# Kernel optimization log

Measured on AMD Instinct MI355X. Metric: run time of the kernel, lower is better.

Reference implementation:

```python
import jax, jax.numpy as jnp
import numpy as np

B, C, H, W = 8, 768, 32, 32
NH = 12
HD = C // NH
HID = 4 * C
EPS = 1e-5


def _layer_norm(x, g, b):
    mu = jnp.mean(x, axis=-1, keepdims=True)
    var = jnp.mean(jnp.square(x - mu), axis=-1, keepdims=True)
    return (x - mu) * jax.lax.rsqrt(var + EPS) * g + b


def setup_inputs() -> dict:
    key = jax.random.key(0)
    ks = jax.random.split(key, 12)
    s = 0.02
    return {
        "x": jax.random.normal(ks[0], (B, C, H, W), jnp.float32),
        "conv_w": jax.random.normal(ks[1], (C, 1, 3, 3), jnp.float32) * s,  # depthwise OIHW
        "conv_b": jnp.zeros((C,), jnp.float32),
        "ln1_g": jnp.ones((C,), jnp.float32),
        "ln1_b": jnp.zeros((C,), jnp.float32),
        "qkv_w": jax.random.normal(ks[2], (3 * C, C), jnp.float32) * s,  # no bias (qkv_bias=False)
        "proj_w": jax.random.normal(ks[3], (C, C), jnp.float32) * s,
        "proj_b": jnp.zeros((C,), jnp.float32),
        "ln2_g": jnp.ones((C,), jnp.float32),
        "ln2_b": jnp.zeros((C,), jnp.float32),
        "fc1_w": jax.random.normal(ks[4], (HID, C), jnp.float32) * s,
        "fc1_b": jnp.zeros((HID,), jnp.float32),
        "fc2_w": jax.random.normal(ks[5], (C, HID), jnp.float32) * s,
        "fc2_b": jnp.zeros((C,), jnp.float32),
    }


def reference(x, conv_w, conv_b, ln1_g, ln1_b, qkv_w, proj_w, proj_b,
              ln2_g, ln2_b, fc1_w, fc1_b, fc2_w, fc2_b):
    # depthwise 3x3 conv positional embedding, residual
    pe = jax.lax.conv_general_dilated(
        x, conv_w, window_strides=(1, 1), padding=((1, 1), (1, 1)),
        dimension_numbers=("NCHW", "OIHW", "NCHW"), feature_group_count=C)
    x = x + pe + conv_b[None, :, None, None]

    b, c, h, w = x.shape
    t = x.reshape(b, c, h * w).transpose(0, 2, 1)  # [B, N, C]

    # attention
    hn = _layer_norm(t, ln1_g, ln1_b)
    qkv = hn @ qkv_w.T  # [B, N, 3C]
    qkv = qkv.reshape(b, h * w, 3, NH, HD).transpose(2, 0, 3, 1, 4)  # [3, B, nh, N, hd]
    q, k, v = qkv[0], qkv[1], qkv[2]
    scale = HD ** -0.5
    attn = jax.nn.softmax(jnp.einsum("bhnd,bhmd->bhnm", q, k) * scale, axis=-1)
    o = jnp.einsum("bhnm,bhmd->bhnd", attn, v).transpose(0, 2, 1, 3).reshape(b, h * w, c)
    t = t + (o @ proj_w.T + proj_b)

    # MLP
    hn = _layer_norm(t, ln2_g, ln2_b)
    hid = jax.nn.gelu(hn @ fc1_w.T + fc1_b, approximate=False)
    t = t + (hid @ fc2_w.T + fc2_b)

    return t.transpose(0, 2, 1).reshape(b, c, h, w)
```

## Files before the change

### kernel.cpp

```cpp
#include <hip/hip_runtime.h>
#include <math.h>


typedef __bf16 bf16;
typedef __attribute__((ext_vector_type(8))) __bf16 bf16x8;
typedef __attribute__((ext_vector_type(4))) __bf16 bf16x4;
typedef __attribute__((ext_vector_type(4))) float f32x4;

#define B_   8
#define C_   768
#define N_   1024
#define NH_  12
#define HD_  64
#define HID_ 3072
#define NTOK   (B_ * N_)
#define NHEADS (B_ * NH_)
#define FA_C   0.1803368801111601f

__device__ __forceinline__ void gload_lds16(const void* g, void* l) {
  __builtin_amdgcn_global_load_lds(
      (__attribute__((address_space(1))) void*)(void*)g,
      (__attribute__((address_space(3))) void*)l, 16, 0, 0);
}

__device__ __forceinline__ float gelu1(float x) {
  float u = 0.7978845608028654f * x * (1.0f + 0.044715f * x * x);
  float e = __builtin_amdgcn_exp2f(u * 2.885390081777927f);
  float th = 1.0f - 2.0f * __builtin_amdgcn_rcpf(e + 1.0f);
  return 0.5f * x * (1.0f + th);
}

#define PIPE_SYNC(N)                                              \
  do {                                                            \
    asm volatile("s_waitcnt vmcnt(" #N ") lgkmcnt(0)" ::: "memory"); \
    __builtin_amdgcn_sched_barrier(0);                            \
    __builtin_amdgcn_s_barrier();                                 \
    __builtin_amdgcn_sched_barrier(0);                            \
    asm volatile("" ::: "memory");                                \
  } while (0)

__global__ __launch_bounds__(512) void gemm_fc1(
    const bf16* __restrict__ A, const bf16* __restrict__ Bw,
    const float* __restrict__ bias, bf16* __restrict__ outp,
    int K, int lda, int ldb, int ntiles, int mtpx, int ldo) {
  __shared__ __align__(16) char smem[114688];
  const int tid = threadIdx.x;
  const int wave = tid >> 6, lane = tid & 63;
  const int wr = wave & 1, wc = wave >> 1;
  const int lr = lane & 15, kq = lane >> 4;

  const int bid = blockIdx.x;
  const int g = bid & 7, s = bid >> 3;
  const int ms = s / ntiles;
  const int m0 = (g * mtpx + ms) * 256;
  const int n0 = (s - ms * ntiles) * 192;

  f32x4 acc[8][3];
#pragma unroll
  for (int i = 0; i < 8; ++i)
#pragma unroll
    for (int j = 0; j < 3; ++j) acc[i][j] = (f32x4){0.f, 0.f, 0.f, 0.f};

  const bf16* pa[4];
  const bf16* pb[3];
  int da[4], db[3];
#pragma unroll
  for (int c = 0; c < 4; ++c) {
    const int sidx = c * 512 + tid;
    const int r = sidx >> 3, seg = (sidx & 7) ^ (r & 7);
    pa[c] = A + (size_t)(m0 + r) * lda + seg * 8;
    da[c] = sidx * 16;
  }
#pragma unroll
  for (int c = 0; c < 3; ++c) {
    const int sidx = c * 512 + tid;
    const int r = sidx >> 3, seg = (sidx & 7) ^ (r & 7);
    pb[c] = Bw + (size_t)(n0 + r) * ldb + seg * 8;
    db[c] = 32768 + sidx * 16;
  }

  const int NT = K >> 6;

  gload_lds16(pb[0], smem + db[0]);
  gload_lds16(pb[1], smem + db[1]);
  gload_lds16(pb[2], smem + db[2]);
  gload_lds16(pa[0], smem + da[0]);
  gload_lds16(pa[1], smem + da[1]);
  gload_lds16(pa[2], smem + da[2]);
  gload_lds16(pa[3], smem + da[3]);
#pragma unroll
  for (int c = 0; c < 4; ++c) pa[c] += 64;
#pragma unroll
  for (int c = 0; c < 3; ++c) pb[c] += 64;

  for (int t = 0; t < NT - 1; ++t) {
    const char* rb = smem + (t & 1) * 57344;
    char* wb = smem + ((t & 1) ^ 1) * 57344;
    bf16x8 af[4], bf0[3], bf1[3];

    PIPE_SYNC(1);
#pragma unroll
    for (int i = 0; i < 4; ++i) {
      const int r = wr * 128 + i * 16 + lr;
      af[i] = *(const bf16x8*)(rb + (r * 8 + (kq ^ (r & 7))) * 16);
    }
#pragma unroll
    for (int j = 0; j < 3; ++j) {
      const int r = wc * 48 + j * 16 + lr;
      bf0[j] = *(const bf16x8*)(rb + 32768 + (r * 8 + (kq ^ (r & 7))) * 16);
    }
    gload_lds16(pb[0], wb + db[0]); pb[0] += 64;
    gload_lds16(pb[1], wb + db[1]); pb[1] += 64;
    __builtin_amdgcn_s_setprio(1);
#pragma unroll
    for (int i = 0; i < 4; ++i)
#pragma unroll
      for (int j = 0; j < 3; ++j)
        acc[i][j] = __builtin_amdgcn_mfma_f32_16x16x32_bf16(bf0[j], af[i],
                                                            acc[i][j], 0, 0, 0);
    __builtin_amdgcn_s_setprio(0);

    PIPE_SYNC(2);
#pragma unroll
    for (int i = 0; i < 4; ++i) {
      const int r = wr * 128 + 64 + i * 16 + lr;
      af[i] = *(const bf16x8*)(rb + (r * 8 + (kq ^ (r & 7))) * 16);
    }
    gload_lds16(pb[2], wb + db[2]); pb[2] += 64;
    gload_lds16(pa[0], wb + da[0]); pa[0] += 64;
    __builtin_amdgcn_s_setprio(1);
#pragma unroll
    for (int i = 0; i < 4; ++i)
#pragma unroll
      for (int j = 0; j < 3; ++j)
        acc[4 + i][j] = __builtin_amdgcn_mfma_f32_16x16x32_bf16(
            bf0[j], af[i], acc[4 + i][j], 0, 0, 0);
    __builtin_amdgcn_s_setprio(0);

    PIPE_SYNC(4);
#pragma unroll
    for (int i = 0; i < 4; ++i) {
      const int r = wr * 128 + i * 16 + lr;
      af[i] = *(const bf16x8*)(rb + (r * 8 + ((4 + kq) ^ (r & 7))) * 16);
    }
#pragma unroll
    for (int j = 0; j < 3; ++j) {
      const int r = wc * 48 + j * 16 + lr;
      bf1[j] = *(const bf16x8*)(rb + 32768 + (r * 8 + ((4 + kq) ^ (r & 7))) * 16);
    }
    gload_lds16(pa[1], wb + da[1]); pa[1] += 64;
    gload_lds16(pa[2], wb + da[2]); pa[2] += 64;
    __builtin_amdgcn_s_setprio(1);
#pragma unroll
    for (int i = 0; i < 4; ++i)
#pragma unroll
      for (int j = 0; j < 3; ++j)
        acc[i][j] = __builtin_amdgcn_mfma_f32_16x16x32_bf16(bf1[j], af[i],
                                                            acc[i][j], 0, 0, 0);
    __builtin_amdgcn_s_setprio(0);

    PIPE_SYNC(6);
#pragma unroll
    for (int i = 0; i < 4; ++i) {
      const int r = wr * 128 + 64 + i * 16 + lr;
      af[i] = *(const bf16x8*)(rb + (r * 8 + ((4 + kq) ^ (r & 7))) * 16);
    }
    gload_lds16(pa[3], wb + da[3]); pa[3] += 64;
    __builtin_amdgcn_s_setprio(1);
#pragma unroll
    for (int i = 0; i < 4; ++i)
#pragma unroll
      for (int j = 0; j < 3; ++j)
        acc[4 + i][j] = __builtin_amdgcn_mfma_f32_16x16x32_bf16(
            bf1[j], af[i], acc[4 + i][j], 0, 0, 0);
    __builtin_amdgcn_s_setprio(0);
  }

  {
    const char* rb = smem + ((NT - 1) & 1) * 57344;
    bf16x8 af[4], bf0[3], bf1[3];
    PIPE_SYNC(0);
#pragma unroll
    for (int j = 0; j < 3; ++j) {
      const int r = wc * 48 + j * 16 + lr;
      bf0[j] = *(const bf16x8*)(rb + 32768 + (r * 8 + (kq ^ (r & 7))) * 16);
      bf1[j] = *(const bf16x8*)(rb + 32768 + (r * 8 + ((4 + kq) ^ (r & 7))) * 16);
    }
    __builtin_amdgcn_s_setprio(1);
#pragma unroll
    for (int half = 0; half < 2; ++half) {
#pragma unroll
      for (int i = 0; i < 4; ++i) {
        const int r = wr * 128 + half * 64 + i * 16 + lr;
        af[i] = *(const bf16x8*)(rb + (r * 8 + (kq ^ (r & 7))) * 16);
      }
#pragma unroll
      for (int i = 0; i < 4; ++i)
#pragma unroll
        for (int j = 0; j < 3; ++j)
          acc[half * 4 + i][j] = __builtin_amdgcn_mfma_f32_16x16x32_bf16(
              bf0[j], af[i], acc[half * 4 + i][j], 0, 0, 0);
#pragma unroll
      for (int i = 0; i < 4; ++i) {
        const int r = wr * 128 + half * 64 + i * 16 + lr;
        af[i] = *(const bf16x8*)(rb + (r * 8 + ((4 + kq) ^ (r & 7))) * 16);
      }
#pragma unroll
      for (int i = 0; i < 4; ++i)
#pragma unroll
        for (int j = 0; j < 3; ++j)
          acc[half * 4 + i][j] = __builtin_amdgcn_mfma_f32_16x16x32_bf16(
              bf1[j], af[i], acc[half * 4 + i][j], 0, 0, 0);
    }
    __builtin_amdgcn_s_setprio(0);
  }

#pragma unroll
  for (int j = 0; j < 3; ++j) {
    const int n = n0 + wc * 48 + j * 16 + kq * 4;
    const f32x4 bv = *(const f32x4*)(bias + n);
#pragma unroll
    for (int i = 0; i < 8; ++i) {
      const int m = m0 + wr * 128 + i * 16 + lr;
      const f32x4 v = acc[i][j];
      bf16x4 pk = {(bf16)gelu1(v[0] + bv[0]), (bf16)gelu1(v[1] + bv[1]),
                   (bf16)gelu1(v[2] + bv[2]), (bf16)gelu1(v[3] + bv[3])};
      *(bf16x4*)(outp + (size_t)m * ldo + n) = pk;
    }
  }
}

__global__ __launch_bounds__(512) void gemm_fc2(
    const bf16* __restrict__ A, const bf16* __restrict__ Bw,
    const float* __restrict__ bias, const float* __restrict__ resid,
    float* __restrict__ outp, int K, int lda, int ldb) {
  __shared__ __align__(16) char smem[122880];
  const int tid = threadIdx.x;
  const int wave = tid >> 6, lane = tid & 63;
  const int wr = wave & 1, wc = wave >> 1;
  const int lr = lane & 15, kq = lane >> 4;

  const int bid = blockIdx.x;
  const int g = bid & 7, s = bid >> 3;
  const int ms = s >> 2;
  const int m0 = (g * 8 + ms) * 128;
  const int n0 = (s & 3) * 192;

  f32x4 acc[4][3];
#pragma unroll
  for (int i = 0; i < 4; ++i)
#pragma unroll
    for (int j = 0; j < 3; ++j) acc[i][j] = (f32x4){0.f, 0.f, 0.f, 0.f};

  const bf16* pa[2];
  const bf16* pb[3];
  int da[2], db[3];
#pragma unroll
  for (int c = 0; c < 2; ++c) {
    const int sidx = c * 512 + tid;
    const int r = sidx >> 3, seg = (sidx & 7) ^ (r & 7);
    pa[c] = A + (size_t)(m0 + r) * lda + seg * 8;
    da[c] = sidx * 16;
  }
#pragma unroll
  for (int c = 0; c < 3; ++c) {
    const int sidx = c * 512 + tid;
    const int r = sidx >> 3, seg = (sidx & 7) ^ (r & 7);
    pb[c] = Bw + (size_t)(n0 + r) * ldb + seg * 8;
    db[c] = 16384 + sidx * 16;
  }

  const int NT = K >> 6;

#pragma unroll
  for (int tt = 0; tt < 2; ++tt) {
    char* wb = smem + tt * 40960;
    gload_lds16(pb[0], wb + db[0]);
    gload_lds16(pb[1], wb + db[1]);
    gload_lds16(pb[2], wb + db[2]);
    gload_lds16(pa[0], wb + da[0]);
    gload_lds16(pa[1], wb + da[1]);
    pb[0] += 64; pb[1] += 64; pb[2] += 64; pa[0] += 64; pa[1] += 64;
  }

  int cur = 0;
  for (int t = 0; t < NT - 1; ++t) {
    const char* rb = smem + cur * 40960;
    PIPE_SYNC(5);
    if (t < NT - 2) {
      int wi = cur + 2; if (wi >= 3) wi -= 3;
      char* wb = smem + wi * 40960;
      gload_lds16(pb[0], wb + db[0]); pb[0] += 64;
      gload_lds16(pb[1], wb + db[1]); pb[1] += 64;
      gload_lds16(pb[2], wb + db[2]); pb[2] += 64;
      gload_lds16(pa[0], wb + da[0]); pa[0] += 64;
      gload_lds16(pa[1], wb + da[1]); pa[1] += 64;
    }
    bf16x8 af[4], bf[3];
#pragma unroll
// ... 13 lines not shown
      for (int j = 0; j < 3; ++j)
        acc[i][j] = __builtin_amdgcn_mfma_f32_16x16x32_bf16(bf[j], af[i],
                                                            acc[i][j], 0, 0, 0);
    __builtin_amdgcn_s_setprio(0);
#pragma unroll
    for (int i = 0; i < 4; ++i) {
      const int r = wr * 64 + i * 16 + lr;
      af[i] = *(const bf16x8*)(rb + (r * 8 + ((4 + kq) ^ (r & 7))) * 16);
    }
#pragma unroll
    for (int j = 0; j < 3; ++j) {
      const int r = wc * 48 + j * 16 + lr;
      bf[j] = *(const bf16x8*)(rb + 16384 + (r * 8 + ((4 + kq) ^ (r & 7))) * 16);
    }
    __builtin_amdgcn_s_setprio(1);
#pragma unroll
    for (int i = 0; i < 4; ++i)
#pragma unroll
      for (int j = 0; j < 3; ++j)
        acc[i][j] = __builtin_amdgcn_mfma_f32_16x16x32_bf16(bf[j], af[i],
                                                            acc[i][j], 0, 0, 0);
    __builtin_amdgcn_s_setprio(0);
    if (++cur == 3) cur = 0;
  }

  {
    const char* rb = smem + cur * 40960;
    bf16x8 af[4], bf[3];
    PIPE_SYNC(0);
#pragma unroll
    for (int kh = 0; kh < 2; ++kh) {
      const int c0 = kh * 4 + kq;
#pragma unroll
      for (int i = 0; i < 4; ++i) {
        const int r = wr * 64 + i * 16 + lr;
        af[i] = *(const bf16x8*)(rb + (r * 8 + (c0 ^ (r & 7))) * 16);
      }
#pragma unroll
      for (int j = 0; j < 3; ++j) {
        const int r = wc * 48 + j * 16 + lr;
        bf[j] = *(const bf16x8*)(rb + 16384 + (r * 8 + (c0 ^ (r & 7))) * 16);
      }
      __builtin_amdgcn_s_setprio(1);
#pragma unroll
      for (int i = 0; i < 4; ++i)
#pragma unroll
        for (int j = 0; j < 3; ++j)
          acc[i][j] = __builtin_amdgcn_mfma_f32_16x16x32_bf16(bf[j], af[i],
                                                              acc[i][j], 0, 0, 0);
      __builtin_amdgcn_s_setprio(0);
    }
  }

  {
    float* tile = (float*)smem;
    const int b = m0 >> 10, tok0 = m0 & (N_ - 1);
#pragma unroll
    for (int sl = 0; sl < 3; ++sl) {
      __syncthreads();
#pragma unroll
      for (int j = 0; j < 3; ++j) {
        const int nl0 = wc * 48 + j * 16 + kq * 4;
        if (((wc * 48 + j * 16) >> 6) == sl) {
          const int n = n0 + nl0;
          const f32x4 bv = *(const f32x4*)(bias + n);
#pragma unroll
          for (int i = 0; i < 4; ++i) {
            const int ml = wr * 64 + i * 16 + lr;
            const float* rp = resid + (size_t)(m0 + ml) * C_ + n;
            f32x4 old = *(const f32x4*)rp;
            const f32x4 v = acc[i][j];
#pragma unroll
            for (int r = 0; r < 4; ++r)
              tile[(nl0 - sl * 64 + r) * 132 + ml] = old[r] + v[r] + bv[r];
          }
        }
      }
      __syncthreads();
      const int nl = tid & 63, mc = tid >> 6;
      float* dst = outp + ((size_t)(b * C_ + n0 + sl * 64 + nl)) * N_ +
                   tok0 + mc * 16;
      const float* src = tile + nl * 132 + mc * 16;
#pragma unroll
      for (int q = 0; q < 4; ++q)
        *(f32x4*)(dst + q * 4) = *(const f32x4*)(src + q * 4);
    }
  }
}

template <int BN, int EPI, bool REMAP>
__global__ __launch_bounds__(256) void gemm_bt(
    const bf16* __restrict__ A, const bf16* __restrict__ B, int K, int lda,
    int ldb, int ntiles, bf16* __restrict__ o0, bf16* __restrict__ o1,
    bf16* __restrict__ o2, float* __restrict__ resid,
    const float* __restrict__ bias, float* __restrict__ outp) {
  constexpr int JJ = BN / 32;
  constexpr int BCH = BN / 32;
  constexpr int STAGE_B = (128 + BN) * 64 * 2;
  constexpr int EXTRA_B = (EPI == 0 ? 128 * 256 : 0);
  constexpr int SMEM_B = STAGE_B > EXTRA_B ? STAGE_B : EXTRA_B;
  __shared__ __align__(16) char smemraw[SMEM_B];
  bf16* As = (bf16*)smemraw;
  bf16* Bs = As + 128 * 64;

  const int tid = threadIdx.x;
  const int wave = tid >> 6, lane = tid & 63;
  const int wm = wave & 1, wn = wave >> 1;
  const int lr = lane & 15, kq = lane >> 4;
  const int sw = lr & 7;

  int m0, n0;
  if constexpr (REMAP) {
    const int bid = blockIdx.x;
    const int g = bid & 7, s = bid >> 3;
    const int ms = s / ntiles;
    m0 = (g * 8 + ms) * 128;
    n0 = (s - ms * ntiles) * BN;
  } else {
    m0 = blockIdx.y * 128;
    n0 = blockIdx.x * BN;
  }

  f32x4 acc[4][JJ];
#pragma unroll
  for (int i = 0; i < 4; i++)
#pragma unroll
    for (int j = 0; j < JJ; j++) acc[i][j] = (f32x4){0.f, 0.f, 0.f, 0.f};

  const bf16* ap[4];
  const bf16* bp[BCH];
  {
    const bf16* Arow = A + (size_t)m0 * lda;
    const bf16* Brow = B + (size_t)n0 * ldb;
#pragma unroll
    for (int it = 0; it < 4; ++it) {
      int s = it * 256 + tid;
      int r = s >> 3, seg = (s & 7) ^ (r & 7);
      ap[it] = Arow + (size_t)r * lda + seg * 8;
    }
#pragma unroll
    for (int it = 0; it < BCH; ++it) {
      int s = it * 256 + tid;
      int r = s >> 3, seg = (s & 7) ^ (r & 7);
      bp[it] = Brow + (size_t)r * ldb + seg * 8;
    }
  }

  for (int k0 = 0; k0 < K; k0 += 64) {
#pragma unroll
    for (int it = 0; it < 4; ++it) {
      gload_lds16(ap[it], (char*)As + (it * 256 + tid) * 16);
      ap[it] += 64;
    }
#pragma unroll
    for (int it = 0; it < BCH; ++it) {
      gload_lds16(bp[it], (char*)Bs + (it * 256 + tid) * 16);
      bp[it] += 64;
    }
    __syncthreads();

#pragma unroll
    for (int h = 0; h < 2; ++h) {
      bf16x8 af[4], bfr[JJ];
      const int c = h * 4 + kq;
#pragma unroll
      for (int i = 0; i < 4; i++) {
        int row = wm * 64 + i * 16 + lr;
        af[i] = *(const bf16x8*)((char*)As + (row * 8 + (c ^ sw)) * 16);
      }
#pragma unroll
      for (int j = 0; j < JJ; j++) {
        int row = wn * (BN / 2) + j * 16 + lr;
        bfr[j] = *(const bf16x8*)((char*)Bs + (row * 8 + (c ^ sw)) * 16);
      }
#pragma unroll
      for (int i = 0; i < 4; i++)
#pragma unroll
        for (int j = 0; j < JJ; j++)
          acc[i][j] = __builtin_amdgcn_mfma_f32_16x16x32_bf16(bfr[j], af[i],
                                                              acc[i][j], 0, 0, 0);
    }
    __syncthreads();
  }

  if constexpr (EPI == 0) {
    const int b = m0 >> 10, tok0 = m0 & (N_ - 1);
    if (n0 < 2 * C_) {
      const int s = n0 >= C_ ? 1 : 0;
      bf16* dst = s ? o1 : o0;
#pragma unroll
      for (int i = 0; i < 4; i++) {
        const int m = m0 + wm * 64 + i * 16 + lr;
#pragma unroll
        for (int j = 0; j < JJ; j++) {
          const int rem = n0 - s * C_ + wn * (BN / 2) + j * 16 + kq * 4;
          const int h = rem >> 6, d = rem & 63;
          const f32x4 v = acc[i][j];
          bf16x4 pk = {(bf16)v[0], (bf16)v[1], (bf16)v[2], (bf16)v[3]};
          size_t head = (size_t)b * NH_ + h;
          *(bf16x4*)(dst + (head * N_ + (m & (N_ - 1))) * HD_ + d) = pk;
        }
      }
    } else {
      bf16* tile = (bf16*)smemraw;
#pragma unroll
      for (int i = 0; i < 4; i++) {
        const int ml = wm * 64 + i * 16 + lr;
        const int mc = ml >> 3, mo = ml & 7;
#pragma unroll
        for (int j = 0; j < JJ; j++) {
          const f32x4 v = acc[i][j];
#pragma unroll
          for (int r = 0; r < 4; r++) {
            const int nl = wn * (BN / 2) + j * 16 + kq * 4 + r;
            *(bf16*)((char*)tile + nl * 256 + ((mc ^ (nl & 15)) * 16) + mo * 2) =
                (bf16)v[r];
          }
        }
      }
      __syncthreads();
      const int nl = tid >> 1, mh = (tid & 1) * 64;
      const int vb = n0 - 2 * C_ + nl;
      const size_t head = (size_t)b * NH_ + (vb >> 6);
      bf16* dst = o2 + (head * HD_ + (vb & 63)) * N_ + tok0 + mh;
#pragma unroll
      for (int c8 = 0; c8 < 8; ++c8) {
        const int c = (mh >> 3) + c8;
        bf16x8 val = *(const bf16x8*)((char*)tile + nl * 256 +
                                      ((c ^ (nl & 15)) * 16));
        *(bf16x8*)(dst + c8 * 8) = val;
      }
    }
  } else if constexpr (EPI == 3) {
#pragma unroll
    for (int j = 0; j < JJ; j++) {
      const int n = n0 + wn * (BN / 2) + j * 16 + kq * 4;
      const f32x4 bv = *(const f32x4*)(bias + n);
#pragma unroll
      for (int i = 0; i < 4; i++) {
        const int m = m0 + wm * 64 + i * 16 + lr;
        float* rp = resid + (size_t)m * C_ + n;
        f32x4 old = *(const f32x4*)rp;
        const f32x4 v = acc[i][j];
        f32x4 nw = {old[0] + v[0] + bv[0], old[1] + v[1] + bv[1],
                    old[2] + v[2] + bv[2], old[3] + v[3] + bv[3]};
        *(f32x4*)rp = nw;
      }
    }
  }
}

__global__ __launch_bounds__(256, 3) void flash_attn(
    const bf16* __restrict__ Qb, const bf16* __restrict__ Kb,
    const bf16* __restrict__ Vt, bf16* __restrict__ attn) {
  __shared__ __align__(16) bf16 ksm[2][64 * 64];
  __shared__ __align__(16) bf16 vsm[2][64 * 64];
  __shared__ __align__(16) bf16 psm[4][32 * 64];

  const int tid = threadIdx.x, wave = tid >> 6, lane = tid & 63;
  const int lr = lane & 15, kq = lane >> 4;
  const int bid = blockIdx.x;
  const int g = bid & 7, s = bid >> 3;
  const int head = g * 12 + (s % 12);
  const int qt = s / 12;
  const int b = head / NH_, hh = head - b * NH_;
  const int q0 = qt * 128;
  const bf16* Qh = Qb + (size_t)head * (N_ * HD_);
  const bf16* Kh = Kb + (size_t)head * (N_ * HD_);
  const bf16* Vh = Vt + (size_t)head * (HD_ * N_);
  char* pw = (char*)&psm[wave][0];

  bf16x8 qf[2][2];
#pragma unroll
  for (int j = 0; j < 2; ++j)
#pragma unroll
    for (int kh = 0; kh < 2; ++kh)
      qf[j][kh] = *(const bf16x8*)(Qh +
                                   (size_t)(q0 + wave * 32 + j * 16 + lr) * HD_ +
                                   kh * 32 + kq * 8);

  f32x4 o[4][2];
#pragma unroll
  for (int i = 0; i < 4; i++)
#pragma unroll
    for (int j = 0; j < 2; j++) o[i][j] = (f32x4){0.f, 0.f, 0.f, 0.f};
  float mprev[2] = {-1e30f, -1e30f}, lacc[2] = {0.f, 0.f};

  auto stage = [&](int t, int bi) {
#pragma unroll
    for (int it = 0; it < 2; ++it) {
      int s2 = it * 256 + tid;
      int r = s2 >> 3, seg = (s2 & 7) ^ (r & 7);
      gload_lds16(Kh + (size_t)(t * 64 + r) * HD_ + seg * 8,
                  (char*)ksm[bi] + (it * 256 + wave * 64) * 16);
    }
#pragma unroll
    for (int it = 0; it < 2; ++it) {
      int s2 = it * 256 + tid;
      int r = s2 >> 3, seg = (s2 & 7) ^ (r & 7);
      gload_lds16(Vh + (size_t)r * N_ + t * 64 + seg * 8,
// ... 169 lines not shown
  float var = rq[0] * (1.f / C_) - mu * mu;
  float rstd = rsqrtf(var + 1e-5f);
  bf16* q = out + (size_t)row * C_;
  q[tid] = (bf16)((v0 - mu) * rstd * g[tid] + be[tid]);
  q[tid + 256] = (bf16)((v1 - mu) * rstd * g[tid + 256] + be[tid + 256]);
  q[tid + 512] = (bf16)((v2 - mu) * rstd * g[tid + 512] + be[tid + 512]);
}

extern "C" void kernel_launch(void* const* d_in, const int* in_sizes, int n_in,
                              void* d_out, int out_size, void* d_ws,
                              size_t ws_size, hipStream_t stream) {
  (void)in_sizes; (void)n_in; (void)out_size; (void)ws_size;
  const float* x      = (const float*)d_in[0];
  const float* conv_w = (const float*)d_in[1];
  const float* conv_b = (const float*)d_in[2];
  const float* ln1_g  = (const float*)d_in[3];
  const float* ln1_b  = (const float*)d_in[4];
  const float* qkv_w  = (const float*)d_in[5];
  const float* proj_w = (const float*)d_in[6];
  const float* proj_b = (const float*)d_in[7];
  const float* ln2_g  = (const float*)d_in[8];
  const float* ln2_b  = (const float*)d_in[9];
  const float* fc1_w  = (const float*)d_in[10];
  const float* fc1_b  = (const float*)d_in[11];
  const float* fc2_w  = (const float*)d_in[12];
  const float* fc2_b  = (const float*)d_in[13];
  float* out = (float*)d_out;

  char* w = (char*)d_ws;
  auto carve = [&](size_t bytes) {
    char* p = w;
    w += (bytes + 255) & ~(size_t)255;
    return p;
  };
  bf16* hid   = (bf16*)carve((size_t)NTOK * HID_ * 2);
  float* t0   = (float*)carve((size_t)NTOK * C_ * 4);
  bf16* lnout = (bf16*)carve((size_t)NTOK * C_ * 2);
  bf16* wq    = (bf16*)carve((size_t)3 * C_ * C_ * 2);
  bf16* wp    = (bf16*)carve((size_t)C_ * C_ * 2);
  bf16* w1    = (bf16*)carve((size_t)HID_ * C_ * 2);
  bf16* w2    = (bf16*)carve((size_t)C_ * HID_ * 2);
  bf16* Qb    = (bf16*)carve((size_t)NHEADS * N_ * HD_ * 2);
  bf16* Kb    = (bf16*)carve((size_t)NHEADS * N_ * HD_ * 2);
  bf16* Vt    = (bf16*)carve((size_t)NHEADS * HD_ * N_ * 2);
  bf16* attn  = (bf16*)carve((size_t)NTOK * C_ * 2);

  const int na = 3 * C_ * C_, nb = C_ * C_, nc = HID_ * C_, nd = C_ * HID_;
  cast_all<<<(na + nb + nc + nd) / 1024, 256, 0, stream>>>(
      qkv_w, na, proj_w, nb, fc1_w, nc, fc2_w, wq);

  conv_pe_t<<<dim3(32, C_ / 32, B_), 256, 0, stream>>>(x, conv_w, conv_b, t0);

  ln_bf16<<<NTOK, 256, 0, stream>>>(t0, ln1_g, ln1_b, lnout);
  gemm_bt<128, 0, true><<<1152, 256, 0, stream>>>(
      lnout, wq, 768, 768, 768, 18, Qb, Kb, Vt, nullptr, nullptr, nullptr);

  flash_attn<<<768, 256, 0, stream>>>(Qb, Kb, Vt, attn);

  gemm_bt<64, 3, true><<<768, 256, 0, stream>>>(
      attn, wp, 768, 768, 768, 12, nullptr, nullptr, nullptr, t0, proj_b,
      nullptr);
  ln_bf16<<<NTOK, 256, 0, stream>>>(t0, ln2_g, ln2_b, lnout);
  gemm_fc1<<<512, 512, 0, stream>>>(lnout, w1, fc1_b, hid, 768, 768, 768,
                                    16, 4, HID_);
  gemm_fc2<<<256, 512, 0, stream>>>(hid, w2, fc2_b, t0, out, 3072, 3072, 3072);
}
```

Baseline: 395.4 us.

## Replace QKV and proj GEMMs with triple-buffered 512-thread pipelined GEMM

Generalizes the fc2-style triple-buffered, 512-thread GEMM into a template with QKV-scatter and residual-add epilogues. It replaces the simple single-buffered 256-thread gemm_bt for the QKV and output-projection GEMMs. The aim is to overlap global-to-LDS loads with MFMA work and to cut barrier stalls. The cost is larger 128x192 tiles, so fewer blocks run (768 for QKV, 256 for proj), which may underfill the GPU for the proj GEMM.

```diff
diff --git a/kernel.cpp b/kernel.cpp
--- a/kernel.cpp
+++ b/kernel.cpp
@@ -39,201 +39,12 @@
     asm volatile("" ::: "memory");                                \
   } while (0)
 
-__global__ __launch_bounds__(512) void gemm_fc1(
-    const bf16* __restrict__ A, const bf16* __restrict__ Bw,
-    const float* __restrict__ bias, bf16* __restrict__ outp,
-    int K, int lda, int ldb, int ntiles, int mtpx, int ldo) {
-  __shared__ __align__(16) char smem[114688];
-  const int tid = threadIdx.x;
-  const int wave = tid >> 6, lane = tid & 63;
-  const int wr = wave & 1, wc = wave >> 1;
-  const int lr = lane & 15, kq = lane >> 4;
-
-  const int bid = blockIdx.x;
-  const int g = bid & 7, s = bid >> 3;
-  const int ms = s / ntiles;
-  const int m0 = (g * mtpx + ms) * 256;
-  const int n0 = (s - ms * ntiles) * 192;
-
-  f32x4 acc[8][3];
-#pragma unroll
-  for (int i = 0; i < 8; ++i)
-#pragma unroll
-    for (int j = 0; j < 3; ++j) acc[i][j] = (f32x4){0.f, 0.f, 0.f, 0.f};
-
-  const bf16* pa[4];
-  const bf16* pb[3];
-  int da[4], db[3];
-#pragma unroll
-  for (int c = 0; c < 4; ++c) {
-    const int sidx = c * 512 + tid;
-    const int r = sidx >> 3, seg = (sidx & 7) ^ (r & 7);
-    pa[c] = A + (size_t)(m0 + r) * lda + seg * 8;
-    da[c] = sidx * 16;
-  }
-#pragma unroll
-  for (int c = 0; c < 3; ++c) {
-    const int sidx = c * 512 + tid;
-    const int r = sidx >> 3, seg = (sidx & 7) ^ (r & 7);
-    pb[c] = Bw + (size_t)(n0 + r) * ldb + seg * 8;
-    db[c] = 32768 + sidx * 16;
-  }
-
-  const int NT = K >> 6;
-
-  gload_lds16(pb[0], smem + db[0]);
-  gload_lds16(pb[1], smem + db[1]);
-  gload_lds16(pb[2], smem + db[2]);
-  gload_lds16(pa[0], smem + da[0]);
-  gload_lds16(pa[1], smem + da[1]);
-  gload_lds16(pa[2], smem + da[2]);
-  gload_lds16(pa[3], smem + da[3]);
-#pragma unroll
-  for (int c = 0; c < 4; ++c) pa[c] += 64;
-#pragma unroll
-  for (int c = 0; c < 3; ++c) pb[c] += 64;
-
-  for (int t = 0; t < NT - 1; ++t) {
-    const char* rb = smem + (t & 1) * 57344;
-    char* wb = smem + ((t & 1) ^ 1) * 57344;
-    bf16x8 af[4], bf0[3], bf1[3];
-
-    PIPE_SYNC(1);
-#pragma unroll
-    for (int i = 0; i < 4; ++i) {
-      const int r = wr * 128 + i * 16 + lr;
-      af[i] = *(const bf16x8*)(rb + (r * 8 + (kq ^ (r & 7))) * 16);
-    }
-#pragma unroll
-    for (int j = 0; j < 3; ++j) {
-      const int r = wc * 48 + j * 16 + lr;
-      bf0[j] = *(const bf16x8*)(rb + 32768 + (r * 8 + (kq ^ (r & 7))) * 16);
-    }
-    gload_lds16(pb[0], wb + db[0]); pb[0] += 64;
-    gload_lds16(pb[1], wb + db[1]); pb[1] += 64;
-    __builtin_amdgcn_s_setprio(1);
-#pragma unroll
-    for (int i = 0; i < 4; ++i)
-#pragma unroll
-      for (int j = 0; j < 3; ++j)
-        acc[i][j] = __builtin_amdgcn_mfma_f32_16x16x32_bf16(bf0[j], af[i],
-                                                            acc[i][j], 0, 0, 0);
-    __builtin_amdgcn_s_setprio(0);
-
-    PIPE_SYNC(2);
-#pragma unroll
-    for (int i = 0; i < 4; ++i) {
-      const int r = wr * 128 + 64 + i * 16 + lr;
-      af[i] = *(const bf16x8*)(rb + (r * 8 + (kq ^ (r & 7))) * 16);
-    }
-    gload_lds16(pb[2], wb + db[2]); pb[2] += 64;
-    gload_lds16(pa[0], wb + da[0]); pa[0] += 64;
-    __builtin_amdgcn_s_setprio(1);
-#pragma unroll
-    for (int i = 0; i < 4; ++i)
-#pragma unroll
-      for (int j = 0; j < 3; ++j)
-        acc[4 + i][j] = __builtin_amdgcn_mfma_f32_16x16x32_bf16(
-            bf0[j], af[i], acc[4 + i][j], 0, 0, 0);
-    __builtin_amdgcn_s_setprio(0);
-
-    PIPE_SYNC(4);
-#pragma unroll
-    for (int i = 0; i < 4; ++i) {
-      const int r = wr * 128 + i * 16 + lr;
-      af[i] = *(const bf16x8*)(rb + (r * 8 + ((4 + kq) ^ (r & 7))) * 16);
-    }
-#pragma unroll
-    for (int j = 0; j < 3; ++j) {
-      const int r = wc * 48 + j * 16 + lr;
-      bf1[j] = *(const bf16x8*)(rb + 32768 + (r * 8 + ((4 + kq) ^ (r & 7))) * 16);
-    }
-    gload_lds16(pa[1], wb + da[1]); pa[1] += 64;
-    gload_lds16(pa[2], wb + da[2]); pa[2] += 64;
-    __builtin_amdgcn_s_setprio(1);
-#pragma unroll
-    for (int i = 0; i < 4; ++i)
-#pragma unroll
-      for (int j = 0; j < 3; ++j)
-        acc[i][j] = __builtin_amdgcn_mfma_f32_16x16x32_bf16(bf1[j], af[i],
-                                                            acc[i][j], 0, 0, 0);
-    __builtin_amdgcn_s_setprio(0);
-
-    PIPE_SYNC(6);
-#pragma unroll
-    for (int i = 0; i < 4; ++i) {
-      const int r = wr * 128 + 64 + i * 16 + lr;
-      af[i] = *(const bf16x8*)(rb + (r * 8 + ((4 + kq) ^ (r & 7))) * 16);
-    }
-    gload_lds16(pa[3], wb + da[3]); pa[3] += 64;
-    __builtin_amdgcn_s_setprio(1);
-#pragma unroll
-    for (int i = 0; i < 4; ++i)
-#pragma unroll
-      for (int j = 0; j < 3; ++j)
-        acc[4 + i][j] = __builtin_amdgcn_mfma_f32_16x16x32_bf16(
-            bf1[j], af[i], acc[4 + i][j], 0, 0, 0);
-    __builtin_amdgcn_s_setprio(0);
-  }
-
-  {
-    const char* rb = smem + ((NT - 1) & 1) * 57344;
-    bf16x8 af[4], bf0[3], bf1[3];
-    PIPE_SYNC(0);
-#pragma unroll
-    for (int j = 0; j < 3; ++j) {
-      const int r = wc * 48 + j * 16 + lr;
-      bf0[j] = *(const bf16x8*)(rb + 32768 + (r * 8 + (kq ^ (r & 7))) * 16);
-      bf1[j] = *(const bf16x8*)(rb + 32768 + (r * 8 + ((4 + kq) ^ (r & 7))) * 16);
-    }
-    __builtin_amdgcn_s_setprio(1);
-#pragma unroll
-    for (int half = 0; half < 2; ++half) {
-#pragma unroll
-      for (int i = 0; i < 4; ++i) {
-        const int r = wr * 128 + half * 64 + i * 16 + lr;
-        af[i] = *(const bf16x8*)(rb + (r * 8 + (kq ^ (r & 7))) * 16);
-      }
-#pragma unroll
-      for (int i = 0; i < 4; ++i)
-#pragma unroll
-        for (int j = 0; j < 3; ++j)
-          acc[half * 4 + i][j] = __builtin_amdgcn_mfma_f32_16x16x32_bf16(
-              bf0[j], af[i], acc[half * 4 + i][j], 0, 0, 0);
-#pragma unroll
-      for (int i = 0; i < 4; ++i) {
-        const int r = wr * 128 + half * 64 + i * 16 + lr;
-        af[i] = *(const bf16x8*)(rb + (r * 8 + ((4 + kq) ^ (r & 7))) * 16);
-      }
-#pragma unroll
-      for (int i = 0; i < 4; ++i)
-#pragma unroll
-        for (int j = 0; j < 3; ++j)
-          acc[half * 4 + i][j] = __builtin_amdgcn_mfma_f32_16x16x32_bf16(
-              bf1[j], af[i], acc[half * 4 + i][j], 0, 0, 0);
-    }
-    __builtin_amdgcn_s_setprio(0);
-  }
-
-#pragma unroll
-  for (int j = 0; j < 3; ++j) {
-    const int n = n0 + wc * 48 + j * 16 + kq * 4;
-    const f32x4 bv = *(const f32x4*)(bias + n);
-#pragma unroll
-    for (int i = 0; i < 8; ++i) {
-      const int m = m0 + wr * 128 + i * 16 + lr;
-      const f32x4 v = acc[i][j];
-      bf16x4 pk = {(bf16)gelu1(v[0] + bv[0]), (bf16)gelu1(v[1] + bv[1]),
-                   (bf16)gelu1(v[2] + bv[2]), (bf16)gelu1(v[3] + bv[3])};
-      *(bf16x4*)(outp + (size_t)m * ldo + n) = pk;
-    }
-  }
-}
-
-__global__ __launch_bounds__(512) void gemm_fc2(
-    const bf16* __restrict__ A, const bf16* __restrict__ Bw,
-    const float* __restrict__ bias, const float* __restrict__ resid,
-    float* __restrict__ outp, int K, int lda, int ldb) {
+template <int EPI>
+__global__ __launch_bounds__(512) void gemm_pipe(
+    const bf16* __restrict__ A, const bf16* __restrict__ Bw, int K, int lda,
+    int ldb, int ntiles, bf16* __restrict__ o0, bf16* __restrict__ o1,
+    bf16* __restrict__ o2, float* __restrict__ resid,
+    const float* __restrict__ bias) {
   __shared__ __align__(16) char smem[122880];
   const int tid = threadIdx.x;
   const int wave = tid >> 6, lane = tid & 63;
@@ -242,9 +53,9 @@
 
   const int bid = blockIdx.x;
   const int g = bid & 7, s = bid >> 3;
-  const int ms = s >> 2;
+  const int ms = s / ntiles;
   const int m0 = (g * 8 + ms) * 128;
-  const int n0 = (s & 3) * 192;
+  const int n0 = (s - ms * ntiles) * 192;
 
   f32x4 acc[4][3];
 #pragma unroll
@@ -364,193 +175,64 @@
     }
   }
 
-  {
-    float* tile = (float*)smem;
-    const int b = m0 >> 10, tok0 = m0 & (N_ - 1);
-#pragma unroll
-    for (int sl = 0; sl < 3; ++sl) {
-      __syncthreads();
-#pragma unroll
-      for (int j = 0; j < 3; ++j) {
-        const int nl0 = wc * 48 + j * 16 + kq * 4;
-        if (((wc * 48 + j * 16) >> 6) == sl) {
-          const int n = n0 + nl0;
-          const f32x4 bv = *(const f32x4*)(bias + n);
-#pragma unroll
-          for (int i = 0; i < 4; ++i) {
-            const int ml = wr * 64 + i * 16 + lr;
-            const float* rp = resid + (size_t)(m0 + ml) * C_ + n;
-            f32x4 old = *(const f32x4*)rp;
-            const f32x4 v = acc[i][j];
-#pragma unroll
-            for (int r = 0; r < 4; ++r)
-              tile[(nl0 - sl * 64 + r) * 132 + ml] = old[r] + v[r] + bv[r];
-          }
-        }
-      }
-      __syncthreads();
-      const int nl = tid & 63, mc = tid >> 6;
-      float* dst = outp + ((size_t)(b * C_ + n0 + sl * 64 + nl)) * N_ +
-                   tok0 + mc * 16;
-      const float* src = tile + nl * 132 + mc * 16;
-#pragma unroll
-      for (int q = 0; q < 4; ++q)
-        *(f32x4*)(dst + q * 4) = *(const f32x4*)(src + q * 4);
-    }
-  }
-}
-
-template <int BN, int EPI, bool REMAP>
-__global__ __launch_bounds__(256) void gemm_bt(
-    const bf16* __restrict__ A, const bf16* __restrict__ B, int K, int lda,
-    int ldb, int ntiles, bf16* __restrict__ o0, bf16* __restrict__ o1,
-    bf16* __restrict__ o2, float* __restrict__ resid,
-    const float* __restrict__ bias, float* __restrict__ outp) {
-  constexpr int JJ = BN / 32;
-  constexpr int BCH = BN / 32;
-  constexpr int STAGE_B = (128 + BN) * 64 * 2;
-  constexpr int EXTRA_B = (EPI == 0 ? 128 * 256 : 0);
-  constexpr int SMEM_B = STAGE_B > EXTRA_B ? STAGE_B : EXTRA_B;
-  __shared__ __align__(16) char smemraw[SMEM_B];
-  bf16* As = (bf16*)smemraw;
-  bf16* Bs = As + 128 * 64;
-
-  const int tid = threadIdx.x;
-  const int wave = tid >> 6, lane = tid & 63;
-  const int wm = wave & 1, wn = wave >> 1;
-  const int lr = lane & 15, kq = lane >> 4;
-  const int sw = lr & 7;
-
-  int m0, n0;
-  if constexpr (REMAP) {
-    const int bid = blockIdx.x;
-    const int g = bid & 7, s = bid >> 3;
-    const int ms = s / ntiles;
-    m0 = (g * 8 + ms) * 128;
-    n0 = (s - ms * ntiles) * BN;
-  } else {
-    m0 = blockIdx.y * 128;
-    n0 = blockIdx.x * BN;
-  }
-
-  f32x4 acc[4][JJ];
-#pragma unroll
-  for (int i = 0; i < 4; i++)
-#pragma unroll
-    for (int j = 0; j < JJ; j++) acc[i][j] = (f32x4){0.f, 0.f, 0.f, 0.f};
-
-  const bf16* ap[4];
-  const bf16* bp[BCH];
-  {
-    const bf16* Arow = A + (size_t)m0 * lda;
-    const bf16* Brow = B + (size_t)n0 * ldb;
-#pragma unroll
-    for (int it = 0; it < 4; ++it) {
-      int s = it * 256 + tid;
-      int r = s >> 3, seg = (s & 7) ^ (r & 7);
-      ap[it] = Arow + (size_t)r * lda + seg * 8;
-    }
-#pragma unroll
-    for (int it = 0; it < BCH; ++it) {
-      int s = it * 256 + tid;
-      int r = s >> 3, seg = (s & 7) ^ (r & 7);
-      bp[it] = Brow + (size_t)r * ldb + seg * 8;
-    }
-  }
-
-  for (int k0 = 0; k0 < K; k0 += 64) {
-#pragma unroll
-    for (int it = 0; it < 4; ++it) {
-      gload_lds16(ap[it], (char*)As + (it * 256 + tid) * 16);
-      ap[it] += 64;
-    }
-#pragma unroll
-    for (int it = 0; it < BCH; ++it) {
-      gload_lds16(bp[it], (char*)Bs + (it * 256 + tid) * 16);
-      bp[it] += 64;
-    }
-    __syncthreads();
-
-#pragma unroll
-    for (int h = 0; h < 2; ++h) {
-      bf16x8 af[4], bfr[JJ];
-      const int c = h * 4 + kq;
-#pragma unroll
-      for (int i = 0; i < 4; i++) {
-        int row = wm * 64 + i * 16 + lr;
-        af[i] = *(const bf16x8*)((char*)As + (row * 8 + (c ^ sw)) * 16);
-      }
-#pragma unroll
-      for (int j = 0; j < JJ; j++) {
-        int row = wn * (BN / 2) + j * 16 + lr;
-        bfr[j] = *(const bf16x8*)((char*)Bs + (row * 8 + (c ^ sw)) * 16);
-      }
-#pragma unroll
-      for (int i = 0; i < 4; i++)
-#pragma unroll
-        for (int j = 0; j < JJ; j++)
-          acc[i][j] = __builtin_amdgcn_mfma_f32_16x16x32_bf16(bfr[j], af[i],
-                                                              acc[i][j], 0, 0, 0);
-    }
-    __syncthreads();
-  }
-
   if constexpr (EPI == 0) {
     const int b = m0 >> 10, tok0 = m0 & (N_ - 1);
     if (n0 < 2 * C_) {
-      const int s = n0 >= C_ ? 1 : 0;
-      bf16* dst = s ? o1 : o0;
-#pragma unroll
-      for (int i = 0; i < 4; i++) {
-        const int m = m0 + wm * 64 + i * 16 + lr;
-#pragma unroll
-        for (int j = 0; j < JJ; j++) {
-          const int rem = n0 - s * C_ + wn * (BN / 2) + j * 16 + kq * 4;
-          const int h = rem >> 6, d = rem & 63;
+      const int sdx = n0 >= C_ ? 1 : 0;
+      bf16* dst = sdx ? o1 : o0;
+      const int nb = n0 - sdx * C_;
+#pragma unroll
+      for (int j = 0; j < 3; ++j) {
+        const int rem = nb + wc * 48 + j * 16 + kq * 4;
+        const int h = rem >> 6, d = rem & 63;
+        bf16* hp = dst + (size_t)(b * NH_ + h) * (N_ * HD_) + d;
+#pragma unroll
+        for (int i = 0; i < 4; ++i) {
+          const int tok = tok0 + wr * 64 + i * 16 + lr;
           const f32x4 v = acc[i][j];
           bf16x4 pk = {(bf16)v[0], (bf16)v[1], (bf16)v[2], (bf16)v[3]};
-          size_t head = (size_t)b * NH_ + h;
-          *(bf16x4*)(dst + (head * N_ + (m & (N_ - 1))) * HD_ + d) = pk;
+          *(bf16x4*)(hp + (size_t)tok * HD_) = pk;
         }
       }
     } else {
-      bf16* tile = (bf16*)smemraw;
-#pragma unroll
-      for (int i = 0; i < 4; i++) {
-        const int ml = wm * 64 + i * 16 + lr;
+      bf16* tile = (bf16*)smem;
+#pragma unroll
+      for (int i = 0; i < 4; ++i) {
+        const int ml = wr * 64 + i * 16 + lr;
         const int mc = ml >> 3, mo = ml & 7;
 #pragma unroll
-        for (int j = 0; j < JJ; j++) {
+        for (int j = 0; j < 3; ++j) {
           const f32x4 v = acc[i][j];
 #pragma unroll
-          for (int r = 0; r < 4; r++) {
-            const int nl = wn * (BN / 2) + j * 16 + kq * 4 + r;
+          for (int r = 0; r < 4; ++r) {
+            const int nl = wc * 48 + j * 16 + kq * 4 + r;
             *(bf16*)((char*)tile + nl * 256 + ((mc ^ (nl & 15)) * 16) + mo * 2) =
                 (bf16)v[r];
           }
         }
       }
       __syncthreads();
-      const int nl = tid >> 1, mh = (tid & 1) * 64;
-      const int vb = n0 - 2 * C_ + nl;
-      const size_t head = (size_t)b * NH_ + (vb >> 6);
-      bf16* dst = o2 + (head * HD_ + (vb & 63)) * N_ + tok0 + mh;
-#pragma unroll
-      for (int c8 = 0; c8 < 8; ++c8) {
-        const int c = (mh >> 3) + c8;
-        bf16x8 val = *(const bf16x8*)((char*)tile + nl * 256 +
-                                      ((c ^ (nl & 15)) * 16));
-        *(bf16x8*)(dst + c8 * 8) = val;
-      }
-    }
-  } else if constexpr (EPI == 3) {
-#pragma unroll
-    for (int j = 0; j < JJ; j++) {
-      const int n = n0 + wn * (BN / 2) + j * 16 + kq * 4;
+      const int vbase = n0 - 2 * C_;
+#pragma unroll
+      for (int c = 0; c < 6; ++c) {
+        const int idx = c * 512 + tid;
+        const int row = idx >> 4, ch = idx & 15;
+        bf16x8 val = *(const bf16x8*)((char*)tile + row * 256 +
+                                      ((ch ^ (row & 15)) * 16));
+        const int vb = vbase + row;
+        bf16* dstp = o2 + ((size_t)(b * NH_ + (vb >> 6)) * HD_ + (vb & 63)) * N_ +
+                     tok0 + ch * 8;
+        *(bf16x8*)dstp = val;
+      }
+    }
+  } else {
+#pragma unroll
+    for (int j = 0; j < 3; ++j) {
+      const int n = n0 + wc * 48 + j * 16 + kq * 4;
       const f32x4 bv = *(const f32x4*)(bias + n);
 #pragma unroll
-      for (int i = 0; i < 4; i++) {
-        const int m = m0 + wm * 64 + i * 16 + lr;
+      for (int i = 0; i < 4; ++i) {
+        const int m = m0 + wr * 64 + i * 16 + lr;
         float* rp = resid + (size_t)m * C_ + n;
         f32x4 old = *(const f32x4*)rp;
         const f32x4 v = acc[i][j];
@@ -558,6 +240,367 @@
                     old[2] + v[2] + bv[2], old[3] + v[3] + bv[3]};
         *(f32x4*)rp = nw;
       }
+    }
+  }
+}
+
+__global__ __launch_bounds__(512) void gemm_fc1(
+    const bf16* __restrict__ A, const bf16* __restrict__ Bw,
+    const float* __restrict__ bias, bf16* __restrict__ outp,
+    int K, int lda, int ldb, int ntiles, int mtpx, int ldo) {
+  __shared__ __align__(16) char smem[114688];
+  const int tid = threadIdx.x;
+  const int wave = tid >> 6, lane = tid & 63;
+  const int wr = wave & 1, wc = wave >> 1;
+  const int lr = lane & 15, kq = lane >> 4;
+
+  const int bid = blockIdx.x;
+  const int g = bid & 7, s = bid >> 3;
+  const int ms = s / ntiles;
+  const int m0 = (g * mtpx + ms) * 256;
+  const int n0 = (s - ms * ntiles) * 192;
+
+  f32x4 acc[8][3];
+#pragma unroll
+  for (int i = 0; i < 8; ++i)
+#pragma unroll
+    for (int j = 0; j < 3; ++j) acc[i][j] = (f32x4){0.f, 0.f, 0.f, 0.f};
+
+  const bf16* pa[4];
+  const bf16* pb[3];
+  int da[4], db[3];
+#pragma unroll
+  for (int c = 0; c < 4; ++c) {
+    const int sidx = c * 512 + tid;
+    const int r = sidx >> 3, seg = (sidx & 7) ^ (r & 7);
+    pa[c] = A + (size_t)(m0 + r) * lda + seg * 8;
+    da[c] = sidx * 16;
+  }
+#pragma unroll
+  for (int c = 0; c < 3; ++c) {
+    const int sidx = c * 512 + tid;
+    const int r = sidx >> 3, seg = (sidx & 7) ^ (r & 7);
+    pb[c] = Bw + (size_t)(n0 + r) * ldb + seg * 8;
+    db[c] = 32768 + sidx * 16;
+  }
+
+  const int NT = K >> 6;
+
+  gload_lds16(pb[0], smem + db[0]);
+  gload_lds16(pb[1], smem + db[1]);
+  gload_lds16(pb[2], smem + db[2]);
+  gload_lds16(pa[0], smem + da[0]);
+  gload_lds16(pa[1], smem + da[1]);
+  gload_lds16(pa[2], smem + da[2]);
+  gload_lds16(pa[3], smem + da[3]);
+#pragma unroll
+  for (int c = 0; c < 4; ++c) pa[c] += 64;
+#pragma unroll
+  for (int c = 0; c < 3; ++c) pb[c] += 64;
+
+  for (int t = 0; t < NT - 1; ++t) {
+    const char* rb = smem + (t & 1) * 57344;
+    char* wb = smem + ((t & 1) ^ 1) * 57344;
+    bf16x8 af[4], bf0[3], bf1[3];
+
+    PIPE_SYNC(1);
+#pragma unroll
+    for (int i = 0; i < 4; ++i) {
+      const int r = wr * 128 + i * 16 + lr;
+      af[i] = *(const bf16x8*)(rb + (r * 8 + (kq ^ (r & 7))) * 16);
+    }
+#pragma unroll
+    for (int j = 0; j < 3; ++j) {
+      const int r = wc * 48 + j * 16 + lr;
+      bf0[j] = *(const bf16x8*)(rb + 32768 + (r * 8 + (kq ^ (r & 7))) * 16);
+    }
+    gload_lds16(pb[0], wb + db[0]); pb[0] += 64;
+    gload_lds16(pb[1], wb + db[1]); pb[1] += 64;
+    __builtin_amdgcn_s_setprio(1);
+#pragma unroll
+    for (int i = 0; i < 4; ++i)
+#pragma unroll
+      for (int j = 0; j < 3; ++j)
+        acc[i][j] = __builtin_amdgcn_mfma_f32_16x16x32_bf16(bf0[j], af[i],
+                                                            acc[i][j], 0, 0, 0);
+    __builtin_amdgcn_s_setprio(0);
+
+    PIPE_SYNC(2);
+#pragma unroll
+    for (int i = 0; i < 4; ++i) {
+      const int r = wr * 128 + 64 + i * 16 + lr;
+      af[i] = *(const bf16x8*)(rb + (r * 8 + (kq ^ (r & 7))) * 16);
+    }
+    gload_lds16(pb[2], wb + db[2]); pb[2] += 64;
+    gload_lds16(pa[0], wb + da[0]); pa[0] += 64;
+    __builtin_amdgcn_s_setprio(1);
+#pragma unroll
+    for (int i = 0; i < 4; ++i)
+#pragma unroll
+      for (int j = 0; j < 3; ++j)
+        acc[4 + i][j] = __builtin_amdgcn_mfma_f32_16x16x32_bf16(
+            bf0[j], af[i], acc[4 + i][j], 0, 0, 0);
+    __builtin_amdgcn_s_setprio(0);
+
+    PIPE_SYNC(4);
+#pragma unroll
+    for (int i = 0; i < 4; ++i) {
+      const int r = wr * 128 + i * 16 + lr;
+      af[i] = *(const bf16x8*)(rb + (r * 8 + ((4 + kq) ^ (r & 7))) * 16);
+    }
+#pragma unroll
+    for (int j = 0; j < 3; ++j) {
+      const int r = wc * 48 + j * 16 + lr;
+      bf1[j] = *(const bf16x8*)(rb + 32768 + (r * 8 + ((4 + kq) ^ (r & 7))) * 16);
+    }
+    gload_lds16(pa[1], wb + da[1]); pa[1] += 64;
+    gload_lds16(pa[2], wb + da[2]); pa[2] += 64;
+    __builtin_amdgcn_s_setprio(1);
+#pragma unroll
+    for (int i = 0; i < 4; ++i)
+#pragma unroll
+      for (int j = 0; j < 3; ++j)
+        acc[i][j] = __builtin_amdgcn_mfma_f32_16x16x32_bf16(bf1[j], af[i],
+                                                            acc[i][j], 0, 0, 0);
+    __builtin_amdgcn_s_setprio(0);
+
+    PIPE_SYNC(6);
+#pragma unroll
+    for (int i = 0; i < 4; ++i) {
+      const int r = wr * 128 + 64 + i * 16 + lr;
+      af[i] = *(const bf16x8*)(rb + (r * 8 + ((4 + kq) ^ (r & 7))) * 16);
+    }
+    gload_lds16(pa[3], wb + da[3]); pa[3] += 64;
+    __builtin_amdgcn_s_setprio(1);
+#pragma unroll
+    for (int i = 0; i < 4; ++i)
+#pragma unroll
+      for (int j = 0; j < 3; ++j)
+        acc[4 + i][j] = __builtin_amdgcn_mfma_f32_16x16x32_bf16(
+            bf1[j], af[i], acc[4 + i][j], 0, 0, 0);
+    __builtin_amdgcn_s_setprio(0);
+  }
+
+  {
+    const char* rb = smem + ((NT - 1) & 1) * 57344;
+    bf16x8 af[4], bf0[3], bf1[3];
+    PIPE_SYNC(0);
+#pragma unroll
+    for (int j = 0; j < 3; ++j) {
+      const int r = wc * 48 + j * 16 + lr;
+      bf0[j] = *(const bf16x8*)(rb + 32768 + (r * 8 + (kq ^ (r & 7))) * 16);
+      bf1[j] = *(const bf16x8*)(rb + 32768 + (r * 8 + ((4 + kq) ^ (r & 7))) * 16);
+    }
+    __builtin_amdgcn_s_setprio(1);
+#pragma unroll
+    for (int half = 0; half < 2; ++half) {
+#pragma unroll
+      for (int i = 0; i < 4; ++i) {
+        const int r = wr * 128 + half * 64 + i * 16 + lr;
+        af[i] = *(const bf16x8*)(rb + (r * 8 + (kq ^ (r & 7))) * 16);
+      }
+#pragma unroll
+      for (int i = 0; i < 4; ++i)
+#pragma unroll
+        for (int j = 0; j < 3; ++j)
+          acc[half * 4 + i][j] = __builtin_amdgcn_mfma_f32_16x16x32_bf16(
+              bf0[j], af[i], acc[half * 4 + i][j], 0, 0, 0);
+#pragma unroll
+      for (int i = 0; i < 4; ++i) {
+        const int r = wr * 128 + half * 64 + i * 16 + lr;
+        af[i] = *(const bf16x8*)(rb + (r * 8 + ((4 + kq) ^ (r & 7))) * 16);
+      }
+#pragma unroll
+      for (int i = 0; i < 4; ++i)
+#pragma unroll
+        for (int j = 0; j < 3; ++j)
+          acc[half * 4 + i][j] = __builtin_amdgcn_mfma_f32_16x16x32_bf16(
+              bf1[j], af[i], acc[half * 4 + i][j], 0, 0, 0);
+    }
+    __builtin_amdgcn_s_setprio(0);
+  }
+
+#pragma unroll
+  for (int j = 0; j < 3; ++j) {
+    const int n = n0 + wc * 48 + j * 16 + kq * 4;
+    const f32x4 bv = *(const f32x4*)(bias + n);
+#pragma unroll
+    for (int i = 0; i < 8; ++i) {
+      const int m = m0 + wr * 128 + i * 16 + lr;
+      const f32x4 v = acc[i][j];
+      bf16x4 pk = {(bf16)gelu1(v[0] + bv[0]), (bf16)gelu1(v[1] + bv[1]),
+                   (bf16)gelu1(v[2] + bv[2]), (bf16)gelu1(v[3] + bv[3])};
+      *(bf16x4*)(outp + (size_t)m * ldo + n) = pk;
+    }
+  }
+}
+
+__global__ __launch_bounds__(512) void gemm_fc2(
+    const bf16* __restrict__ A, const bf16* __restrict__ Bw,
+    const float* __restrict__ bias, const float* __restrict__ resid,
+    float* __restrict__ outp, int K, int lda, int ldb) {
+  __shared__ __align__(16) char smem[122880];
+  const int tid = threadIdx.x;
+  const int wave = tid >> 6, lane = tid & 63;
+  const int wr = wave & 1, wc = wave >> 1;
+  const int lr = lane & 15, kq = lane >> 4;
+
+  const int bid = blockIdx.x;
+  const int g = bid & 7, s = bid >> 3;
+  const int ms = s >> 2;
+  const int m0 = (g * 8 + ms) * 128;
+  const int n0 = (s & 3) * 192;
+
+  f32x4 acc[4][3];
+#pragma unroll
+  for (int i = 0; i < 4; ++i)
+#pragma unroll
+    for (int j = 0; j < 3; ++j) acc[i][j] = (f32x4){0.f, 0.f, 0.f, 0.f};
+
+  const bf16* pa[2];
+  const bf16* pb[3];
+  int da[2], db[3];
+#pragma unroll
+  for (int c = 0; c < 2; ++c) {
+    const int sidx = c * 512 + tid;
+    const int r = sidx >> 3, seg = (sidx & 7) ^ (r & 7);
+    pa[c] = A + (size_t)(m0 + r) * lda + seg * 8;
+    da[c] = sidx * 16;
+  }
+#pragma unroll
+  for (int c = 0; c < 3; ++c) {
+    const int sidx = c * 512 + tid;
+    const int r = sidx >> 3, seg = (sidx & 7) ^ (r & 7);
+    pb[c] = Bw + (size_t)(n0 + r) * ldb + seg * 8;
+    db[c] = 16384 + sidx * 16;
+  }
+
+  const int NT = K >> 6;
+
+#pragma unroll
+  for (int tt = 0; tt < 2; ++tt) {
+    char* wb = smem + tt * 40960;
+    gload_lds16(pb[0], wb + db[0]);
+    gload_lds16(pb[1], wb + db[1]);
+    gload_lds16(pb[2], wb + db[2]);
+    gload_lds16(pa[0], wb + da[0]);
+    gload_lds16(pa[1], wb + da[1]);
+    pb[0] += 64; pb[1] += 64; pb[2] += 64; pa[0] += 64; pa[1] += 64;
+  }
+
+  int cur = 0;
+  for (int t = 0; t < NT - 1; ++t) {
+    const char* rb = smem + cur * 40960;
+    PIPE_SYNC(5);
+    if (t < NT - 2) {
+      int wi = cur + 2; if (wi >= 3) wi -= 3;
+      char* wb = smem + wi * 40960;
+      gload_lds16(pb[0], wb + db[0]); pb[0] += 64;
+      gload_lds16(pb[1], wb + db[1]); pb[1] += 64;
+      gload_lds16(pb[2], wb + db[2]); pb[2] += 64;
+      gload_lds16(pa[0], wb + da[0]); pa[0] += 64;
+      gload_lds16(pa[1], wb + da[1]); pa[1] += 64;
+    }
+    bf16x8 af[4], bf[3];
+#pragma unroll
+    for (int i = 0; i < 4; ++i) {
+      const int r = wr * 64 + i * 16 + lr;
+      af[i] = *(const bf16x8*)(rb + (r * 8 + (kq ^ (r & 7))) * 16);
+    }
+#pragma unroll
+    for (int j = 0; j < 3; ++j) {
+      const int r = wc * 48 + j * 16 + lr;
+      bf[j] = *(const bf16x8*)(rb + 16384 + (r * 8 + (kq ^ (r & 7))) * 16);
+    }
+    __builtin_amdgcn_s_setprio(1);
+#pragma unroll
+    for (int i = 0; i < 4; ++i)
+#pragma unroll
+      for (int j = 0; j < 3; ++j)
+        acc[i][j] = __builtin_amdgcn_mfma_f32_16x16x32_bf16(bf[j], af[i],
+                                                            acc[i][j], 0, 0, 0);
+    __builtin_amdgcn_s_setprio(0);
+#pragma unroll
+    for (int i = 0; i < 4; ++i) {
+      const int r = wr * 64 + i * 16 + lr;
+      af[i] = *(const bf16x8*)(rb + (r * 8 + ((4 + kq) ^ (r & 7))) * 16);
+    }
+#pragma unroll
+    for (int j = 0; j < 3; ++j) {
+      const int r = wc * 48 + j * 16 + lr;
+      bf[j] = *(const bf16x8*)(rb + 16384 + (r * 8 + ((4 + kq) ^ (r & 7))) * 16);
+    }
+    __builtin_amdgcn_s_setprio(1);
+#pragma unroll
+    for (int i = 0; i < 4; ++i)
+#pragma unroll
+      for (int j = 0; j < 3; ++j)
+        acc[i][j] = __builtin_amdgcn_mfma_f32_16x16x32_bf16(bf[j], af[i],
+                                                            acc[i][j], 0, 0, 0);
+    __builtin_amdgcn_s_setprio(0);
+    if (++cur == 3) cur = 0;
+  }
+
+  {
+    const char* rb = smem + cur * 40960;
+    bf16x8 af[4], bf[3];
+    PIPE_SYNC(0);
+#pragma unroll
+    for (int kh = 0; kh < 2; ++kh) {
+      const int c0 = kh * 4 + kq;
+#pragma unroll
+      for (int i = 0; i < 4; ++i) {
+        const int r = wr * 64 + i * 16 + lr;
+        af[i] = *(const bf16x8*)(rb + (r * 8 + (c0 ^ (r & 7))) * 16);
+      }
+#pragma unroll
+      for (int j = 0; j < 3; ++j) {
+        const int r = wc * 48 + j * 16 + lr;
+        bf[j] = *(const bf16x8*)(rb + 16384 + (r * 8 + (c0 ^ (r & 7))) * 16);
+      }
+      __builtin_amdgcn_s_setprio(1);
+#pragma unroll
+      for (int i = 0; i < 4; ++i)
+#pragma unroll
+        for (int j = 0; j < 3; ++j)
+          acc[i][j] = __builtin_amdgcn_mfma_f32_16x16x32_bf16(bf[j], af[i],
+                                                              acc[i][j], 0, 0, 0);
+      __builtin_amdgcn_s_setprio(0);
+    }
+  }
+
+  {
+    float* tile = (float*)smem;
+    const int b = m0 >> 10, tok0 = m0 & (N_ - 1);
+#pragma unroll
+    for (int sl = 0; sl < 3; ++sl) {
+      __syncthreads();
+#pragma unroll
+      for (int j = 0; j < 3; ++j) {
+        const int nl0 = wc * 48 + j * 16 + kq * 4;
+        if (((wc * 48 + j * 16) >> 6) == sl) {
+          const int n = n0 + nl0;
+          const f32x4 bv = *(const f32x4*)(bias + n);
+#pragma unroll
+          for (int i = 0; i < 4; ++i) {
+            const int ml = wr * 64 + i * 16 + lr;
+            const float* rp = resid + (size_t)(m0 + ml) * C_ + n;
+            f32x4 old = *(const f32x4*)rp;
+            const f32x4 v = acc[i][j];
+#pragma unroll
+            for (int r = 0; r < 4; ++r)
+              tile[(nl0 - sl * 64 + r) * 132 + ml] = old[r] + v[r] + bv[r];
+          }
+        }
+      }
+      __syncthreads();
+      const int nl = tid & 63, mc = tid >> 6;
+      float* dst = outp + ((size_t)(b * C_ + n0 + sl * 64 + nl)) * N_ +
+                   tok0 + mc * 16;
+      const float* src = tile + nl * 132 + mc * 16;
+#pragma unroll
+      for (int q = 0; q < 4; ++q)
+        *(f32x4*)(dst + q * 4) = *(const f32x4*)(src + q * 4);
     }
   }
 }
@@ -833,14 +876,13 @@
   conv_pe_t<<<dim3(32, C_ / 32, B_), 256, 0, stream>>>(x, conv_w, conv_b, t0);
 
   ln_bf16<<<NTOK, 256, 0, stream>>>(t0, ln1_g, ln1_b, lnout);
-  gemm_bt<128, 0, true><<<1152, 256, 0, stream>>>(
-      lnout, wq, 768, 768, 768, 18, Qb, Kb, Vt, nullptr, nullptr, nullptr);
+  gemm_pipe<0><<<768, 512, 0, stream>>>(lnout, wq, 768, 768, 768, 12,
+                                        Qb, Kb, Vt, nullptr, nullptr);
 
   flash_attn<<<768, 256, 0, stream>>>(Qb, Kb, Vt, attn);
 
-  gemm_bt<64, 3, true><<<768, 256, 0, stream>>>(
-      attn, wp, 768, 768, 768, 12, nullptr, nullptr, nullptr, t0, proj_b,
-      nullptr);
+  gemm_pipe<1><<<256, 512, 0, stream>>>(attn, wp, 768, 768, 768, 4,
+                                        nullptr, nullptr, nullptr, t0, proj_b);
   ln_bf16<<<NTOK, 256, 0, stream>>>(t0, ln2_g, ln2_b, lnout);
   gemm_fc1<<<512, 512, 0, stream>>>(lnout, w1, fc1_b, hid, 768, 768, 768,
                                     16, 4, HID_);
```

New measurement: 382.8 us (median of 2 runs). -3.2%, faster.
